# Kernel tuning notes

Hardware: AMD Instinct MI355X
Metric: run time of the kernel (lower is better)

Reference implementation:

```python
import jax, jax.numpy as jnp
import numpy as np

B, S, D, DFF, H, V, L = 2, 1024, 1024, 4096, 16, 32000, 8
DH = D // H
EPS = 1e-5

def _pe():
    pos = np.arange(S, dtype=np.float32)[:, None]
    div = np.exp(np.arange(0, D, 2, dtype=np.float32) * (-np.log(10000.0) / D))
    pe = np.zeros((S, D), dtype=np.float32)
    pe[:, 0::2] = np.sin(pos * div)
    pe[:, 1::2] = np.cos(pos * div)
    return jnp.asarray(pe)

PE = _pe()

def _ln(h, g, b):
    m = jnp.mean(h, axis=-1, keepdims=True)
    v = jnp.mean((h - m) ** 2, axis=-1, keepdims=True)
    return (h - m) * jax.lax.rsqrt(v + EPS) * g + b

def setup_inputs():
    key = jax.random.key(0)
    k = jax.random.split(key, 16)
    sc = 0.02
    return {
        'x': jax.random.randint(k[0], (B, S), 0, V),
        'mask': jnp.tril(jnp.ones((1, 1, S, S), dtype=bool)),
        'emb': jax.random.normal(k[1], (V, D)) * sc,
        'Wq': jax.random.normal(k[2], (L, D, D)) * sc,
        'Wk': jax.random.normal(k[3], (L, D, D)) * sc,
        'Wv': jax.random.normal(k[4], (L, D, D)) * sc,
        'Wo': jax.random.normal(k[5], (L, D, D)) * sc,
        'ln1_g': jnp.ones((L, D)), 'ln1_b': jnp.zeros((L, D)),
        'ln2_g': jnp.ones((L, D)), 'ln2_b': jnp.zeros((L, D)),
        'W1': jax.random.normal(k[6], (L, D, DFF)) * sc,
        'b1': jnp.zeros((L, DFF)),
        'W2': jax.random.normal(k[7], (L, DFF, D)) * sc,
        'b2': jnp.zeros((L, D)),
        'lnf_g': jnp.ones((D,)), 'lnf_b': jnp.zeros((D,)),
        'projW': jax.random.normal(k[8], (D, V)) * sc,
        'projb': jnp.zeros((V,)),
    }

def reference(x, mask, emb, Wq, Wk, Wv, Wo, ln1_g, ln1_b, ln2_g, ln2_b,
              W1, b1, W2, b2, lnf_g, lnf_b, projW, projb):
    # embedding * sqrt(D) + positional encoding
    h = emb[x] * jnp.sqrt(jnp.float32(D)) + PE[None, :, :]
    scale = 1.0 / jnp.sqrt(jnp.float32(DH))
    for i in range(L):
        # --- self-attention sublayer (pre-LN residual) ---
        a_in = _ln(h, ln1_g[i], ln1_b[i])
        q = (a_in @ Wq[i]).reshape(B, S, H, DH)
        kk = (a_in @ Wk[i]).reshape(B, S, H, DH)
        v = (a_in @ Wv[i]).reshape(B, S, H, DH)
        scores = jnp.einsum('bqhd,bkhd->bhqk', q, kk) * scale
        scores = jnp.where(mask, scores, -1e9)
        attn = jax.nn.softmax(scores, axis=-1)
        o = jnp.einsum('bhqk,bkhd->bqhd', attn, v).reshape(B, S, D)
        h = h + o @ Wo[i]
        # --- feed-forward sublayer ---
        f_in = _ln(h, ln2_g[i], ln2_b[i])
        h = h + (jax.nn.relu(f_in @ W1[i] + b1[i]) @ W2[i] + b2[i])
    h = _ln(h, lnf_g, lnf_b)
    return h @ projW + projb
```

## Files before the change

kernel.cpp:

```cpp
#include <hip/hip_runtime.h>

typedef __bf16 bf16;
typedef __bf16 bf16x4 __attribute__((ext_vector_type(4)));
typedef __bf16 bf16x8 __attribute__((ext_vector_type(8)));
typedef float f32x4 __attribute__((ext_vector_type(4)));
typedef short short4v __attribute__((ext_vector_type(4)));

__device__ __forceinline__ short f2bs(float x) {
  bf16 hv = (bf16)x;
  return __builtin_bit_cast(short, hv);
}

__device__ __forceinline__ void gl_lds16(const void* g, void* l) {
  __builtin_amdgcn_global_load_lds(
      (const __attribute__((address_space(1))) unsigned int*)g,
      (__attribute__((address_space(3))) unsigned int*)l, 16, 0, 0);
}

__global__ __launch_bounds__(256) void wt_k(const float* __restrict__ in,
    bf16* __restrict__ out, int K, int N, long in_ls, long out_ls)
{
  __shared__ float t[64][33];
  const int z = blockIdx.z;
  const float* ip = in + (size_t)z * in_ls;
  bf16* op = out + (size_t)z * out_ls;
  const int n0 = blockIdx.x * 32, k0 = blockIdx.y * 64;
  const int tid = threadIdx.x;
  const int kr = tid >> 3, nc = (tid & 7) * 4;
#pragma unroll
  for (int hh = 0; hh < 2; ++hh) {
    float4 v = *(const float4*)(ip + (size_t)(k0 + kr + hh * 32) * N + n0 + nc);
    t[kr + hh * 32][nc]     = v.x;
    t[kr + hh * 32][nc + 1] = v.y;
    t[kr + hh * 32][nc + 2] = v.z;
    t[kr + hh * 32][nc + 3] = v.w;
  }
  __syncthreads();
  const int nr = tid >> 3, kc = (tid & 7) * 8;
  bf16x8 o;
#pragma unroll
  for (int j = 0; j < 8; ++j) o[j] = (bf16)t[kc + j][nr];
  *(bf16x8*)(op + (size_t)(n0 + nr) * K + k0 + kc) = o;
}

__global__ __launch_bounds__(256) void embed_k(const int* __restrict__ x,
    const float* __restrict__ emb, float* __restrict__ h)
{
  const int m = blockIdx.x, t = threadIdx.x;
  const int s = m & 1023;
  const int tok = x[m];
  const int d0 = t * 4;
  float4 e = *(const float4*)(emb + (size_t)tok * 1024 + d0);
  const float* ep = &e.x;
  float r[4];
#pragma unroll
  for (int j = 0; j < 4; ++j) {
    int d = d0 + j;
    float freq = expf((float)(d & ~1) * (-9.2103403719761836f / 1024.f));
    float ang = (float)s * freq;
    float pe = (d & 1) ? cosf(ang) : sinf(ang);
    r[j] = ep[j] * 32.f + pe;
  }
  *(float4*)(h + (size_t)m * 1024 + d0) = make_float4(r[0], r[1], r[2], r[3]);
}

__global__ __launch_bounds__(256) void ln_k(const float* __restrict__ h,
    const float* __restrict__ g, const float* __restrict__ b,
    bf16* __restrict__ out)
{
  const int row = blockIdx.x, t = threadIdx.x;
  const float* hr = h + (size_t)row * 1024;
  float4 x = *(const float4*)(hr + t * 4);
  float s  = x.x + x.y + x.z + x.w;
  float ss = x.x * x.x + x.y * x.y + x.z * x.z + x.w * x.w;
#pragma unroll
  for (int off = 32; off >= 1; off >>= 1) {
    s  += __shfl_down(s, off);
    ss += __shfl_down(ss, off);
  }
  __shared__ float sb[4], ssb[4];
  if ((t & 63) == 0) { sb[t >> 6] = s; ssb[t >> 6] = ss; }
  __syncthreads();
  s  = sb[0] + sb[1] + sb[2] + sb[3];
  ss = ssb[0] + ssb[1] + ssb[2] + ssb[3];
  const float mean = s * (1.f / 1024.f);
  const float var  = ss * (1.f / 1024.f) - mean * mean;
  const float rstd = rsqrtf(var + 1e-5f);
  const float* xp = &x.x;
#pragma unroll
  for (int j = 0; j < 4; ++j) {
    int d = t * 4 + j;
    out[(size_t)row * 1024 + d] = (bf16)((xp[j] - mean) * rstd * g[d] + b[d]);
  }
}

__global__ __launch_bounds__(1024) void gemm256_k(
    const bf16* __restrict__ A, const bf16* __restrict__ Bt,
    const float* __restrict__ bias, float* __restrict__ C,
    int M, int N, int K)
{
  __shared__ __align__(16) bf16 As[2][256 * 64];
  __shared__ __align__(16) bf16 Bs[2][256 * 64];

  const int nwg = gridDim.x;
  const int orig = blockIdx.x;
  const int q8 = nwg >> 3, r8 = nwg & 7;
  const int xcd = orig & 7, loc = orig >> 3;
  const int wg = (xcd < r8 ? xcd * (q8 + 1) : r8 * (q8 + 1) + (xcd - r8) * q8) + loc;
  const int nrowt = M >> 8;
  const int rowt = wg & (nrowt - 1);
  const int colt = wg / nrowt;
  const int m0 = rowt * 256;
  const int n0 = colt * 256;
  const int nt = K >> 6;

  const int tid = threadIdx.x;
  const int lane = tid & 63;
  const int wbase = tid & ~63;
  const int wid = tid >> 6;
  const int wm = wid >> 2, wn = wid & 3;
  const int qr = lane & 15, grp = lane >> 4;

  f32x4 acc[4][4];
#pragma unroll
  for (int i = 0; i < 4; ++i)
#pragma unroll
    for (int j = 0; j < 4; ++j) acc[i][j] = (f32x4){0.f, 0.f, 0.f, 0.f};

  auto stage = [&](int bufi, int kt) {
#pragma unroll
    for (int it = 0; it < 2; ++it) {
      const int idx = it * 1024 + tid;
      const int row = idx >> 3, c = idx & 7;
      const int bo = (c * 16) ^ ((row & 7) << 4);
      gl_lds16((const char*)(A + (size_t)(m0 + row) * K + kt) + bo,
               (char*)&As[bufi][0] + (size_t)(it * 1024 + wbase) * 16);
    }
#pragma unroll
    for (int it = 0; it < 2; ++it) {
      const int idx = it * 1024 + tid;
      const int row = idx >> 3, c = idx & 7;
      const int bo = (c * 16) ^ ((row & 7) << 4);
      gl_lds16((const char*)(Bt + (size_t)(n0 + row) * K + kt) + bo,
               (char*)&Bs[bufi][0] + (size_t)(it * 1024 + wbase) * 16);
    }
  };

  stage(0, 0);
  for (int t = 0; t < nt; ++t) {
    const int cur = t & 1;
    if (t + 1 < nt) {
      stage(cur ^ 1, (t + 1) * 64);
      asm volatile("s_waitcnt vmcnt(4)" ::: "memory");
    } else {
      asm volatile("s_waitcnt vmcnt(0)" ::: "memory");
    }
    __builtin_amdgcn_s_barrier();
    asm volatile("" ::: "memory");
#pragma unroll
    for (int ks = 0; ks < 2; ++ks) {
      bf16x8 af[4], bfr[4];
#pragma unroll
      for (int mi = 0; mi < 4; ++mi) {
        const int arow = wm * 64 + mi * 16 + qr;
        const int ab = arow * 128 + ((grp * 16 + ks * 64) ^ ((arow & 7) << 4));
        af[mi] = *(const bf16x8*)((const char*)&As[cur][0] + ab);
      }
#pragma unroll
      for (int ni = 0; ni < 4; ++ni) {
        const int brow = wn * 64 + ni * 16 + qr;
        const int bb = brow * 128 + ((grp * 16 + ks * 64) ^ ((brow & 7) << 4));
        bfr[ni] = *(const bf16x8*)((const char*)&Bs[cur][0] + bb);
      }
      __builtin_amdgcn_s_setprio(1);
#pragma unroll
      for (int mi = 0; mi < 4; ++mi)
#pragma unroll
        for (int ni = 0; ni < 4; ++ni)
          acc[mi][ni] = __builtin_amdgcn_mfma_f32_16x16x32_bf16(
              bfr[ni], af[mi], acc[mi][ni], 0, 0, 0);
      __builtin_amdgcn_s_setprio(0);
    }
    __builtin_amdgcn_s_barrier();
    asm volatile("" ::: "memory");
  }

#pragma unroll
  for (int mi = 0; mi < 4; ++mi) {
    const int rowg = m0 + wm * 64 + mi * 16 + qr;
#pragma unroll
    for (int ni = 0; ni < 4; ++ni) {
      const int colg = n0 + wn * 64 + ni * 16 + grp * 4;
      float4 bv = *(const float4*)(bias + colg);
      float4 o;
      o.x = acc[mi][ni][0] + bv.x;
      o.y = acc[mi][ni][1] + bv.y;
      o.z = acc[mi][ni][2] + bv.z;
      o.w = acc[mi][ni][3] + bv.w;
      *(float4*)(C + (size_t)rowg * N + colg) = o;
    }
  }
}

template<int MODE, int NSPLIT>
__global__ __launch_bounds__(256) void gemm3_k(
    const bf16* __restrict__ A, const bf16* __restrict__ Bt,
    const float* __restrict__ bias, void* __restrict__ Cout,
    float* __restrict__ Hacc, bf16* __restrict__ Vt,
    int M, int N, int K)
{
  __shared__ __align__(16) bf16 As[2][128 * 64];
  __shared__ __align__(16) bf16 Bs[2][128 * 64];

  const int nwg = gridDim.x;
  const int orig = blockIdx.x;
  const int q8 = nwg >> 3, r8 = nwg & 7;
  const int xcd = orig & 7, loc = orig >> 3;
  const int wg = (xcd < r8 ? xcd * (q8 + 1) : r8 * (q8 + 1) + (xcd - r8) * q8) + loc;
  const int nrowt = M >> 7;
  const int ntiles = nrowt * (N >> 7);
  const int split = (NSPLIT > 1) ? (wg / ntiles) : 0;
  const int tile  = (NSPLIT > 1) ? (wg % ntiles) : wg;
  const int rowt = tile & (nrowt - 1);
  const int colt = tile / nrowt;
  const int m0 = rowt * 128;
  const int n0 = colt * 128;
  const int Ks = K / NSPLIT;
  const int k_begin = split * Ks;
  const int nt = Ks >> 6;

  const int tid = threadIdx.x;
  const int lane = tid & 63;
  const int wbase = tid & ~63;
  const int wid = tid >> 6;
  const int wm = wid >> 1, wn = wid & 1;
  const int qr = lane & 15, grp = lane >> 4;

  f32x4 acc[4][4];
#pragma unroll
  for (int i = 0; i < 4; ++i)
#pragma unroll
    for (int j = 0; j < 4; ++j) acc[i][j] = (f32x4){0.f, 0.f, 0.f, 0.f};

  auto stage = [&](int bufi, int kt) {
#pragma unroll
    for (int it = 0; it < 4; ++it) {
      const int idx = it * 256 + tid;
      const int row = idx >> 3, c = idx & 7;
      const int bo = (c * 16) ^ ((row & 7) << 4);
      gl_lds16((const char*)(A + (size_t)(m0 + row) * K + kt) + bo,
               (char*)&As[bufi][0] + (size_t)(it * 256 + wbase) * 16);
    }
#pragma unroll
    for (int it = 0; it < 4; ++it) {
      const int idx = it * 256 + tid;
      const int row = idx >> 3, c = idx & 7;
      const int bo = (c * 16) ^ ((row & 7) << 4);
      gl_lds16((const char*)(Bt + (size_t)(n0 + row) * K + kt) + bo,
               (char*)&Bs[bufi][0] + (size_t)(it * 256 + wbase) * 16);
    }
  };

  stage(0, k_begin);
  for (int t = 0; t < nt; ++t) {
    const int cur = t & 1;
    if (t + 1 < nt) {
      stage(cur ^ 1, k_begin + (t + 1) * 64);
      asm volatile("s_waitcnt vmcnt(8)" ::: "memory");
    } else {
      asm volatile("s_waitcnt vmcnt(0)" ::: "memory");
    }
    __builtin_amdgcn_s_barrier();
    asm volatile("" ::: "memory");
#pragma unroll
    for (int ks = 0; ks < 2; ++ks) {
      bf16x8 af[4], bfr[4];
#pragma unroll
      for (int mi = 0; mi < 4; ++mi) {
        const int arow = wm * 64 + mi * 16 + qr;
        const int ab = arow * 128 + ((grp * 16 + ks * 64) ^ ((arow & 7) << 4));
        af[mi] = *(const bf16x8*)((const char*)&As[cur][0] + ab);
      }
#pragma unroll
      for (int ni = 0; ni < 4; ++ni) {
        const int brow = wn * 64 + ni * 16 + qr;
        const int bb = brow * 128 + ((grp * 16 + ks * 64) ^ ((brow & 7) << 4));
        bfr[ni] = *(const bf16x8*)((const char*)&Bs[cur][0] + bb);
      }
      __builtin_amdgcn_s_setprio(1);
#pragma unroll
      for (int mi = 0; mi < 4; ++mi)
#pragma unroll
        for (int ni = 0; ni < 4; ++ni)
          acc[mi][ni] = __builtin_amdgcn_mfma_f32_16x16x32_bf16(
              af[mi], bfr[ni], acc[mi][ni], 0, 0, 0);
      __builtin_amdgcn_s_setprio(0);
    }
    __builtin_amdgcn_s_barrier();
    asm volatile("" ::: "memory");
  }

  const int sel = (MODE == 5) ? (n0 >> 10) : 0;
#pragma unroll
  for (int ni = 0; ni < 4; ++ni) {
    const int coln = wn * 64 + ni * 16 + qr;
    const int colg = n0 + coln;
    float bv = 0.f;
    if (MODE == 1) bv = bias[colg];
    if (MODE == 3 && split == 0) bv = bias[colg];
#pragma unroll
    for (int mi = 0; mi < 4; ++mi) {
      const int rowg0 = m0 + wm * 64 + mi * 16 + grp * 4;
      if (MODE == 5 && sel == 2) {
        const int b = rowg0 >> 10, s = rowg0 & 1023;
        bf16x4 pv;
#pragma unroll
        for (int r = 0; r < 4; ++r) pv[r] = (bf16)acc[mi][ni][r];
        *(bf16x4*)(Vt + (size_t)b * 1024 * 1024 + (size_t)(colg & 1023) * 1024 + s) = pv;
      } else {
#pragma unroll
        for (int r = 0; r < 4; ++r) {
          const int rowg = rowg0 + r;
          float v = acc[mi][ni][r];
          if (MODE == 1) {
            v += bv; v = v > 0.f ? v : 0.f;
            ((bf16*)Cout)[(size_t)rowg * N + colg] = (bf16)v;
          } else if (MODE == 2) {
            if (NSPLIT > 1) atomicAdd(&Hacc[(size_t)rowg * N + colg], v);
            else            Hacc[(size_t)rowg * N + colg] += v;
          } else if (MODE == 3) {
            if (NSPLIT > 1) atomicAdd(&Hacc[(size_t)rowg * N + colg], v + bv);
            else            Hacc[(size_t)rowg * N + colg] += v + bv;
          } else if (MODE == 5) {
            bf16* cb = (bf16*)Cout + (size_t)sel * 2048 * 1024;
            cb[(size_t)rowg * 1024 + (colg & 1023)] = (bf16)v;
          }
        }
      }
    }
  }
}

__global__ __launch_bounds__(64) void attn_k(const bf16* __restrict__ qm,
    const bf16* __restrict__ km, const bf16* __restrict__ vt,
    bf16* __restrict__ om)
{
  const int lane = threadIdx.x;
  const int qr = lane & 15, g = lane >> 4;
  const int qt = blockIdx.x & 63;
  const int hh = (blockIdx.x >> 6) & 15;
  const int bb = blockIdx.x >> 10;
  const size_t rowb = (size_t)bb * 1024;
  const int hb = hh * 64;

  const bf16* qp = qm + (rowb + qt * 16 + qr) * 1024 + hb + g * 8;
  const bf16x8 qf0 = *(const bf16x8*)qp;
  const bf16x8 qf1 = *(const bf16x8*)(qp + 32);

  float m_run = -1e30f, l_run = 0.f;
  f32x4 oacc[4];
#pragma unroll
  for (int dt = 0; dt < 4; ++dt) oacc[dt] = (f32x4){0.f, 0.f, 0.f, 0.f};

  const int qglob = qt * 16 + qr;
  const bf16* vtb = vt + (size_t)bb * 1024 * 1024;
  const bf16* kbase = km + rowb * 1024 + hb;

  auto tile_step = [&](int kvt, bool masked) {
    const bf16* kp = kbase + (size_t)kvt * 16 * 1024 + qr * 1024 + g * 8;
    bf16x8 kf0 = *(const bf16x8*)kp;
    bf16x8 kf1 = *(const bf16x8*)(kp + 32);
    bf16x4 vf[4];
#pragma unroll
    for (int dt = 0; dt < 4; ++dt)
      vf[dt] = *(const bf16x4*)(vtb + (size_t)(hb + dt * 16 + qr) * 1024 + kvt * 16 + g * 4);
    f32x4 st = (f32x4){0.f, 0.f, 0.f, 0.f};
    st = __builtin_amdgcn_mfma_f32_16x16x32_bf16(kf0, qf0, st, 0, 0, 0);
    st = __builtin_amdgcn_mfma_f32_16x16x32_bf16(kf1, qf1, st, 0, 0, 0);
    float sc[4];
#pragma unroll
    for (int r = 0; r < 4; ++r) {
      sc[r] = st[r] * 0.125f;
      if (masked && (kvt * 16 + g * 4 + r > qglob)) sc[r] = -1e30f;
    }
    float mloc = fmaxf(fmaxf(sc[0], sc[1]), fmaxf(sc[2], sc[3]));
    mloc = fmaxf(mloc, __shfl_xor(mloc, 16));
    mloc = fmaxf(mloc, __shfl_xor(mloc, 32));
    float m_new = fmaxf(m_run, mloc);
    float alpha = __expf(m_run - m_new);
    float p[4], ps = 0.f;
#pragma unroll
    for (int r = 0; r < 4; ++r) { p[r] = __expf(sc[r] - m_new); ps += p[r]; }
    ps += __shfl_xor(ps, 16);
    ps += __shfl_xor(ps, 32);
    l_run = l_run * alpha + ps;
    m_run = m_new;
    short4v pfa;
#pragma unroll
    for (int r = 0; r < 4; ++r) pfa[r] = f2bs(p[r]);
#pragma unroll
    for (int dt = 0; dt < 4; ++dt) {
      oacc[dt] *= alpha;
      oacc[dt] = __builtin_amdgcn_mfma_f32_16x16x16bf16_1k(
          __builtin_bit_cast(short4v, vf[dt]), pfa, oacc[dt], 0, 0, 0);
    }
  };

  const int nun = qt;
  int kvt = 0;
  for (; kvt + 1 < nun; kvt += 2) {
    const bf16* kpa = kbase + (size_t)kvt * 16 * 1024 + qr * 1024 + g * 8;
    const bf16* kpb = kpa + 16 * 1024;
    bf16x8 ka0 = *(const bf16x8*)kpa;
    bf16x8 ka1 = *(const bf16x8*)(kpa + 32);
    bf16x8 kb0 = *(const bf16x8*)kpb;
    bf16x8 kb1 = *(const bf16x8*)(kpb + 32);
    bf16x4 vfa[4], vfb[4];
#pragma unroll
    for (int dt = 0; dt < 4; ++dt) {
      const bf16* vp = vtb + (size_t)(hb + dt * 16 + qr) * 1024 + kvt * 16 + g * 4;
      vfa[dt] = *(const bf16x4*)vp;
      vfb[dt] = *(const bf16x4*)(vp + 16);
    }
    f32x4 sa = (f32x4){0.f, 0.f, 0.f, 0.f};
    f32x4 sb = (f32x4){0.f, 0.f, 0.f, 0.f};
    sa = __builtin_amdgcn_mfma_f32_16x16x32_bf16(ka0, qf0, sa, 0, 0, 0);
    sb = __builtin_amdgcn_mfma_f32_16x16x32_bf16(kb0, qf0, sb, 0, 0, 0);
    sa = __builtin_amdgcn_mfma_f32_16x16x32_bf16(ka1, qf1, sa, 0, 0, 0);
    sb = __builtin_amdgcn_mfma_f32_16x16x32_bf16(kb1, qf1, sb, 0, 0, 0);
    float pa[4], pb[4];
    float mloc = -1e30f;
#pragma unroll
    for (int r = 0; r < 4; ++r) {
      pa[r] = sa[r] * 0.125f; pb[r] = sb[r] * 0.125f;
      mloc = fmaxf(mloc, fmaxf(pa[r], pb[r]));
    }
    mloc = fmaxf(mloc, __shfl_xor(mloc, 16));
    mloc = fmaxf(mloc, __shfl_xor(mloc, 32));
    float m_new = fmaxf(m_run, mloc);
    float alpha = __expf(m_run - m_new);
    float ps = 0.f;
#pragma unroll
    for (int r = 0; r < 4; ++r) {
      pa[r] = __expf(pa[r] - m_new); pb[r] = __expf(pb[r] - m_new);
      ps += pa[r] + pb[r];
    }
    ps += __shfl_xor(ps, 16);
    ps += __shfl_xor(ps, 32);
    l_run = l_run * alpha + ps;
    m_run = m_new;
    short4v pfa, pfb;
#pragma unroll
    for (int r = 0; r < 4; ++r) { pfa[r] = f2bs(pa[r]); pfb[r] = f2bs(pb[r]); }
#pragma unroll
    for (int dt = 0; dt < 4; ++dt) {
      oacc[dt] *= alpha;
      oacc[dt] = __builtin_amdgcn_mfma_f32_16x16x16bf16_1k(
          __builtin_bit_cast(short4v, vfa[dt]), pfa, oacc[dt], 0, 0, 0);
      oacc[dt] = __builtin_amdgcn_mfma_f32_16x16x16bf16_1k(
          __builtin_bit_cast(short4v, vfb[dt]), pfb, oacc[dt], 0, 0, 0);
    }
  }
  for (; kvt < nun; ++kvt) tile_step(kvt, false);
  tile_step(qt, true);

  const float inv = 1.f / l_run;
  bf16* op = om + (rowb + qt * 16 + qr) * 1024 + hb;
#pragma unroll
  for (int dt = 0; dt < 4; ++dt)
#pragma unroll
    for (int r = 0; r < 4; ++r)
      op[dt * 16 + g * 4 + r] = (bf16)(oacc[dt][r] * inv);
}

extern "C" void kernel_launch(void* const* d_in, const int* in_sizes, int n_in,
                              void* d_out, int out_size, void* d_ws, size_t ws_size,
                              hipStream_t stream)
{
  (void)in_sizes; (void)n_in; (void)out_size; (void)ws_size;
  const int*   x     = (const int*)d_in[0];
  const float* emb   = (const float*)d_in[2];
  const float* Wq    = (const float*)d_in[3];
  const float* Wk    = (const float*)d_in[4];
  const float* Wv    = (const float*)d_in[5];
  const float* Wo    = (const float*)d_in[6];
  const float* ln1g  = (const float*)d_in[7];
  const float* ln1b  = (const float*)d_in[8];
  const float* ln2g  = (const float*)d_in[9];
  const float* ln2b  = (const float*)d_in[10];
  const float* W1    = (const float*)d_in[11];
  const float* b1    = (const float*)d_in[12];
  const float* W2    = (const float*)d_in[13];
  const float* b2    = (const float*)d_in[14];
  const float* lnfg  = (const float*)d_in[15];
  const float* lnfb  = (const float*)d_in[16];
  const float* projW = (const float*)d_in[17];
  const float* projb = (const float*)d_in[18];

  char* ws = (char*)d_ws;
  const size_t MB = 1u << 20;
  float* h    = (float*)(ws + 0);
  bf16*  ain  = (bf16*)(ws + 8 * MB);
  bf16*  qb   = (bf16*)(ws + 12 * MB);
  bf16*  kb   = (bf16*)(ws + 16 * MB);
  bf16*  vtb  = (bf16*)(ws + 20 * MB);
  bf16*  ob   = (bf16*)(ws + 24 * MB);
  bf16*  mid  = (bf16*)(ws + 28 * MB);
  bf16*  Bqkv = (bf16*)(ws + 44 * MB);
  bf16*  Bo   = (bf16*)(ws + 92 * MB);
  bf16*  B1t  = (bf16*)(ws + 108 * MB);
  bf16*  B2t  = (bf16*)(ws + 172 * MB);
  bf16*  Bprj = (bf16*)(ws + 236 * MB);

  const long M1 = 1024 * 1024, M3 = 3 * M1, M4 = 4 * M1;

  wt_k<<<dim3(32, 16, 8),   256, 0, stream>>>(Wq, Bqkv,          1024, 1024, M1, M3);
  wt_k<<<dim3(32, 16, 8),   256, 0, stream>>>(Wk, Bqkv + M1,     1024, 1024, M1, M3);
  wt_k<<<dim3(32, 16, 8),   256, 0, stream>>>(Wv, Bqkv + 2 * M1, 1024, 1024, M1, M3);
  wt_k<<<dim3(32, 16, 8),   256, 0, stream>>>(Wo, Bo,            1024, 1024, M1, M1);
  wt_k<<<dim3(128, 16, 8),  256, 0, stream>>>(W1, B1t,           1024, 4096, M4, M4);
  wt_k<<<dim3(32, 64, 8),   256, 0, stream>>>(W2, B2t,           4096, 1024, M4, M4);
  wt_k<<<dim3(1000, 16, 1), 256, 0, stream>>>(projW, Bprj,       1024, 32000, 0, 0);

  embed_k<<<dim3(2048), 256, 0, stream>>>(x, emb, h);
  for (int i = 0; i < 8; ++i) {
    ln_k<<<dim3(2048), 256, 0, stream>>>(h, ln1g + i * 1024, ln1b + i * 1024, ain);
    gemm3_k<5,1><<<dim3(384), 256, 0, stream>>>(ain, Bqkv + i * M3, nullptr,
                                                qb, nullptr, vtb, 2048, 3072, 1024);
    attn_k<<<dim3(2048), 64, 0, stream>>>(qb, kb, vtb, ob);
    gemm3_k<2,2><<<dim3(256), 256, 0, stream>>>(ob, Bo + i * M1, nullptr,
                                                nullptr, h, nullptr, 2048, 1024, 1024);
    ln_k<<<dim3(2048), 256, 0, stream>>>(h, ln2g + i * 1024, ln2b + i * 1024, ain);
    gemm3_k<1,1><<<dim3(512), 256, 0, stream>>>(ain, B1t + i * M4, b1 + i * 4096,
                                                mid, nullptr, nullptr, 2048, 4096, 1024);
    gemm3_k<3,2><<<dim3(256), 256, 0, stream>>>(mid, B2t + i * M4, b2 + i * 1024,
                                                nullptr, h, nullptr, 2048, 1024, 4096);
  }
  ln_k<<<dim3(2048), 256, 0, stream>>>(h, lnfg, lnfb, ain);
  gemm256_k<<<dim3(1000), 1024, 0, stream>>>(ain, Bprj, projb,
                                             (float*)d_out, 2048, 32000, 1024);
}
```

Measured before the change: 2.149 ms.

## Halve GEMM K-tile to 32 and route vocab projection through 128x128 kernel

The generic 128x128 GEMM kernel now stages 32-wide K slices instead of 64, with a 4-row XOR swizzle and half the LDS per buffer. The 256x256 1024-thread projection kernel is removed, and the vocabulary projection runs through a new MODE 4 of the 128x128 kernel that writes a float4 epilogue with bias. The smaller LDS footprint may let more workgroups share a CU, but each tile now takes twice as many barrier-separated iterations. The projection's smaller tiles also give less operand reuse per loaded byte.

```diff
diff --git a/kernel.cpp b/kernel.cpp
--- a/kernel.cpp
+++ b/kernel.cpp
@@ -94,114 +94,6 @@
   }
 }
 
-__global__ __launch_bounds__(1024) void gemm256_k(
-    const bf16* __restrict__ A, const bf16* __restrict__ Bt,
-    const float* __restrict__ bias, float* __restrict__ C,
-    int M, int N, int K)
-{
-  __shared__ __align__(16) bf16 As[2][256 * 64];
-  __shared__ __align__(16) bf16 Bs[2][256 * 64];
-
-  const int nwg = gridDim.x;
-  const int orig = blockIdx.x;
-  const int q8 = nwg >> 3, r8 = nwg & 7;
-  const int xcd = orig & 7, loc = orig >> 3;
-  const int wg = (xcd < r8 ? xcd * (q8 + 1) : r8 * (q8 + 1) + (xcd - r8) * q8) + loc;
-  const int nrowt = M >> 8;
-  const int rowt = wg & (nrowt - 1);
-  const int colt = wg / nrowt;
-  const int m0 = rowt * 256;
-  const int n0 = colt * 256;
-  const int nt = K >> 6;
-
-  const int tid = threadIdx.x;
-  const int lane = tid & 63;
-  const int wbase = tid & ~63;
-  const int wid = tid >> 6;
-  const int wm = wid >> 2, wn = wid & 3;
-  const int qr = lane & 15, grp = lane >> 4;
-
-  f32x4 acc[4][4];
-#pragma unroll
-  for (int i = 0; i < 4; ++i)
-#pragma unroll
-    for (int j = 0; j < 4; ++j) acc[i][j] = (f32x4){0.f, 0.f, 0.f, 0.f};
-
-  auto stage = [&](int bufi, int kt) {
-#pragma unroll
-    for (int it = 0; it < 2; ++it) {
-      const int idx = it * 1024 + tid;
-      const int row = idx >> 3, c = idx & 7;
-      const int bo = (c * 16) ^ ((row & 7) << 4);
-      gl_lds16((const char*)(A + (size_t)(m0 + row) * K + kt) + bo,
-               (char*)&As[bufi][0] + (size_t)(it * 1024 + wbase) * 16);
-    }
-#pragma unroll
-    for (int it = 0; it < 2; ++it) {
-      const int idx = it * 1024 + tid;
-      const int row = idx >> 3, c = idx & 7;
-      const int bo = (c * 16) ^ ((row & 7) << 4);
-      gl_lds16((const char*)(Bt + (size_t)(n0 + row) * K + kt) + bo,
-               (char*)&Bs[bufi][0] + (size_t)(it * 1024 + wbase) * 16);
-    }
-  };
-
-  stage(0, 0);
-  for (int t = 0; t < nt; ++t) {
-    const int cur = t & 1;
-    if (t + 1 < nt) {
-      stage(cur ^ 1, (t + 1) * 64);
-      asm volatile("s_waitcnt vmcnt(4)" ::: "memory");
-    } else {
-      asm volatile("s_waitcnt vmcnt(0)" ::: "memory");
-    }
-    __builtin_amdgcn_s_barrier();
-    asm volatile("" ::: "memory");
-#pragma unroll
-    for (int ks = 0; ks < 2; ++ks) {
-      bf16x8 af[4], bfr[4];
-#pragma unroll
-      for (int mi = 0; mi < 4; ++mi) {
-        const int arow = wm * 64 + mi * 16 + qr;
-        const int ab = arow * 128 + ((grp * 16 + ks * 64) ^ ((arow & 7) << 4));
-        af[mi] = *(const bf16x8*)((const char*)&As[cur][0] + ab);
-      }
-#pragma unroll
-      for (int ni = 0; ni < 4; ++ni) {
-        const int brow = wn * 64 + ni * 16 + qr;
-        const int bb = brow * 128 + ((grp * 16 + ks * 64) ^ ((brow & 7) << 4));
-        bfr[ni] = *(const bf16x8*)((const char*)&Bs[cur][0] + bb);
-      }
-      __builtin_amdgcn_s_setprio(1);
-#pragma unroll
-      for (int mi = 0; mi < 4; ++mi)
-#pragma unroll
-        for (int ni = 0; ni < 4; ++ni)
-          acc[mi][ni] = __builtin_amdgcn_mfma_f32_16x16x32_bf16(
-              bfr[ni], af[mi], acc[mi][ni], 0, 0, 0);
-      __builtin_amdgcn_s_setprio(0);
-    }
-    __builtin_amdgcn_s_barrier();
-    asm volatile("" ::: "memory");
-  }
-
-#pragma unroll
-  for (int mi = 0; mi < 4; ++mi) {
-    const int rowg = m0 + wm * 64 + mi * 16 + qr;
-#pragma unroll
-    for (int ni = 0; ni < 4; ++ni) {
-      const int colg = n0 + wn * 64 + ni * 16 + grp * 4;
-      float4 bv = *(const float4*)(bias + colg);
-      float4 o;
-      o.x = acc[mi][ni][0] + bv.x;
-      o.y = acc[mi][ni][1] + bv.y;
-      o.z = acc[mi][ni][2] + bv.z;
-      o.w = acc[mi][ni][3] + bv.w;
-      *(float4*)(C + (size_t)rowg * N + colg) = o;
-    }
-  }
-}
-
 template<int MODE, int NSPLIT>
 __global__ __launch_bounds__(256) void gemm3_k(
     const bf16* __restrict__ A, const bf16* __restrict__ Bt,
@@ -209,8 +101,8 @@
     float* __restrict__ Hacc, bf16* __restrict__ Vt,
     int M, int N, int K)
 {
-  __shared__ __align__(16) bf16 As[2][128 * 64];
-  __shared__ __align__(16) bf16 Bs[2][128 * 64];
+  __shared__ __align__(16) bf16 As[2][128 * 32];
+  __shared__ __align__(16) bf16 Bs[2][128 * 32];
 
   const int nwg = gridDim.x;
   const int orig = blockIdx.x;
@@ -227,7 +119,7 @@
   const int n0 = colt * 128;
   const int Ks = K / NSPLIT;
   const int k_begin = split * Ks;
-  const int nt = Ks >> 6;
+  const int nt = Ks >> 5;
 
   const int tid = threadIdx.x;
   const int lane = tid & 63;
@@ -244,18 +136,18 @@
 
   auto stage = [&](int bufi, int kt) {
 #pragma unroll
-    for (int it = 0; it < 4; ++it) {
+    for (int it = 0; it < 2; ++it) {
       const int idx = it * 256 + tid;
-      const int row = idx >> 3, c = idx & 7;
-      const int bo = (c * 16) ^ ((row & 7) << 4);
+      const int row = idx >> 2, c = idx & 3;
+      const int bo = (c * 16) ^ ((row & 3) << 4);
       gl_lds16((const char*)(A + (size_t)(m0 + row) * K + kt) + bo,
                (char*)&As[bufi][0] + (size_t)(it * 256 + wbase) * 16);
     }
 #pragma unroll
-    for (int it = 0; it < 4; ++it) {
+    for (int it = 0; it < 2; ++it) {
       const int idx = it * 256 + tid;
-      const int row = idx >> 3, c = idx & 7;
-      const int bo = (c * 16) ^ ((row & 7) << 4);
+      const int row = idx >> 2, c = idx & 3;
+      const int bo = (c * 16) ^ ((row & 3) << 4);
       gl_lds16((const char*)(Bt + (size_t)(n0 + row) * K + kt) + bo,
                (char*)&Bs[bufi][0] + (size_t)(it * 256 + wbase) * 16);
     }
@@ -265,39 +157,60 @@
   for (int t = 0; t < nt; ++t) {
     const int cur = t & 1;
     if (t + 1 < nt) {
-      stage(cur ^ 1, k_begin + (t + 1) * 64);
-      asm volatile("s_waitcnt vmcnt(8)" ::: "memory");
+      stage(cur ^ 1, k_begin + (t + 1) * 32);
+      asm volatile("s_waitcnt vmcnt(4)" ::: "memory");
     } else {
       asm volatile("s_waitcnt vmcnt(0)" ::: "memory");
     }
     __builtin_amdgcn_s_barrier();
     asm volatile("" ::: "memory");
-#pragma unroll
-    for (int ks = 0; ks < 2; ++ks) {
-      bf16x8 af[4], bfr[4];
-#pragma unroll
-      for (int mi = 0; mi < 4; ++mi) {
-        const int arow = wm * 64 + mi * 16 + qr;
-        const int ab = arow * 128 + ((grp * 16 + ks * 64) ^ ((arow & 7) << 4));
-        af[mi] = *(const bf16x8*)((const char*)&As[cur][0] + ab);
-      }
+    bf16x8 af[4], bfr[4];
+#pragma unroll
+    for (int mi = 0; mi < 4; ++mi) {
+      const int arow = wm * 64 + mi * 16 + qr;
+      const int ab = arow * 64 + ((grp * 16) ^ ((arow & 3) << 4));
+      af[mi] = *(const bf16x8*)((const char*)&As[cur][0] + ab);
+    }
+#pragma unroll
+    for (int ni = 0; ni < 4; ++ni) {
+      const int brow = wn * 64 + ni * 16 + qr;
+      const int bb = brow * 64 + ((grp * 16) ^ ((brow & 3) << 4));
+      bfr[ni] = *(const bf16x8*)((const char*)&Bs[cur][0] + bb);
+    }
+    __builtin_amdgcn_s_setprio(1);
+#pragma unroll
+    for (int mi = 0; mi < 4; ++mi)
 #pragma unroll
       for (int ni = 0; ni < 4; ++ni) {
-        const int brow = wn * 64 + ni * 16 + qr;
-        const int bb = brow * 128 + ((grp * 16 + ks * 64) ^ ((brow & 7) << 4));
-        bfr[ni] = *(const bf16x8*)((const char*)&Bs[cur][0] + bb);
-      }
-      __builtin_amdgcn_s_setprio(1);
-#pragma unroll
-      for (int mi = 0; mi < 4; ++mi)
-#pragma unroll
-        for (int ni = 0; ni < 4; ++ni)
+        if (MODE == 4)
+          acc[mi][ni] = __builtin_amdgcn_mfma_f32_16x16x32_bf16(
+              bfr[ni], af[mi], acc[mi][ni], 0, 0, 0);
+        else
           acc[mi][ni] = __builtin_amdgcn_mfma_f32_16x16x32_bf16(
               af[mi], bfr[ni], acc[mi][ni], 0, 0, 0);
-      __builtin_amdgcn_s_setprio(0);
-    }
+      }
+    __builtin_amdgcn_s_setprio(0);
     __builtin_amdgcn_s_barrier();
     asm volatile("" ::: "memory");
+  }
+
+  if (MODE == 4) {
+#pragma unroll
+    for (int mi = 0; mi < 4; ++mi) {
+      const int rowg = m0 + wm * 64 + mi * 16 + qr;
+#pragma unroll
+      for (int ni = 0; ni < 4; ++ni) {
+        const int colg = n0 + wn * 64 + ni * 16 + grp * 4;
+        float4 bv = *(const float4*)(bias + colg);
+        float4 o;
+        o.x = acc[mi][ni][0] + bv.x;
+        o.y = acc[mi][ni][1] + bv.y;
+        o.z = acc[mi][ni][2] + bv.z;
+        o.w = acc[mi][ni][3] + bv.w;
+        *(float4*)((float*)Cout + (size_t)rowg * N + colg) = o;
+      }
+    }
+    return;
   }
 
   const int sel = (MODE == 5) ? (n0 >> 10) : 0;
@@ -537,6 +450,6 @@
                                                 nullptr, h, nullptr, 2048, 1024, 4096);
   }
   ln_k<<<dim3(2048), 256, 0, stream>>>(h, lnfg, lnfb, ain);
-  gemm256_k<<<dim3(1000), 1024, 0, stream>>>(ain, Bprj, projb,
-                                             (float*)d_out, 2048, 32000, 1024);
-}
+  gemm3_k<4,1><<<dim3(4000), 256, 0, stream>>>(ain, Bprj, projb,
+                                               d_out, nullptr, nullptr, 2048, 32000, 1024);
+}
```

After: 2.348 ms. 1.09x slower.
